# Optimization experiments

Hardware: AMD Instinct MI355X
Metric: run time of the kernel (lower is better)

The kernel has to match this reference:

```python
import jax, jax.numpy as jnp
import numpy as np

SIZE = 8
MAX_NOISY_RATIO = 0.1
MAX_WEIGHT_RATIO = 1.0


def setup_inputs() -> dict:
    key = jax.random.key(0)
    k1, k2, k3 = jax.random.split(key, 3)
    b, c, h, w = 32, 1, 128, 128
    H, W = h * SIZE, w * SIZE
    return {
        "dmap_conv": jax.random.uniform(k1, (b, c, h, w), jnp.float32),
        "dmap_tran": jax.random.uniform(k2, (b, c, h, w), jnp.float32),
        "gt_density": jax.random.uniform(k3, (b, c, H, W), jnp.float32),
        "process": 1,
    }


def reference(dmap_conv, dmap_tran, gt_density, process):
    b, c, h, w = dmap_conv.shape
    weight = MAX_WEIGHT_RATIO * process
    noisy_ratio = MAX_NOISY_RATIO * process

    # AvgPool2d(kernel=SIZE) * SIZE^2 == sum over non-overlapping SIZE x SIZE blocks
    gt = gt_density.reshape(b, c, h, SIZE, w, SIZE).sum(axis=(3, 5))  # [b,c,h,w]

    dc = dmap_conv.reshape(b, -1)  # [b, c*h*w]
    dt = dmap_tran.reshape(b, -1)
    dg = gt.reshape(b, -1)

    num = int(h * w * noisy_ratio)
    if num < 1:
        return jnp.sum((dc - dg) ** 2) + jnp.sum((dt - dg) ** 2)

    err_c = jnp.abs(dg - dc)
    err_t = jnp.abs(dg - dt)
    comb_c = weight * dc + (1.0 - weight) * dg
    comb_t = weight * dt + (1.0 - weight) * dg

    # threshold = num-th largest error per row (min of top-k)
    thr_c = jax.lax.top_k(err_c, num)[0][:, -1:]  # [b,1]
    sup_from_tran = jnp.where(err_c >= thr_c, comb_t, dg)
    mse_conv = jnp.sum((dc - sup_from_tran) ** 2)

    thr_t = jax.lax.top_k(err_t, num)[0][:, -1:]
    sup_from_conv = jnp.where(err_t >= thr_t, comb_c, dg)
    mse_tran = jnp.sum((dt - sup_from_conv) ** 2)

    return mse_conv + mse_tran
```

## Files before the change

kernel.cpp:

```cpp
#include <hip/hip_runtime.h>
#include <hip/hip_bf16.h>

#define B 32
#define HW 16384
#define NROW 128
#define POOL 8
#define GTW 1024
#define TOTAL (B * HW)
#define LOSS_BLOCKS 1024

__global__ __launch_bounds__(256) void pool_kernel(const float* __restrict__ gt,
                                                   float* __restrict__ dg) {
    int out = blockIdx.x * 256 + threadIdx.x;
    int b   = out >> 14;
    int rem = out & (HW - 1);
    int oi  = rem >> 7;
    int oj  = rem & (NROW - 1);
    const float* base = gt + ((size_t)b << 20) + (size_t)(oi * POOL) * GTW + oj * POOL;
    float s = 0.f;
#pragma unroll
    for (int r = 0; r < POOL; ++r) {
        const float4* p = reinterpret_cast<const float4*>(base + (size_t)r * GTW);
        float4 a = p[0];
        float4 c = p[1];
        s += a.x + a.y + a.z + a.w + c.x + c.y + c.z + c.w;
    }
    dg[out] = s;
}

__global__ __launch_bounds__(256) void select_kernel(const float* __restrict__ dc_all,
                                                     const float* __restrict__ dt_all,
                                                     const float* __restrict__ dg_all,
                                                     const int* __restrict__ process,
                                                     float* __restrict__ thr_out) {
    int b     = blockIdx.x >> 1;
    int which = blockIdx.x & 1;
    const float* dm = (which ? dt_all : dc_all) + (size_t)b * HW;
    const float* dg = dg_all + (size_t)b * HW;

    int p = process[0];
    int num = (int)(16384.0 * (0.1 * (double)p));
    if (num > HW) num = HW;

    int t = threadIdx.x;

    if (num < 1) {
        if (t == 0) thr_out[which * B + b] = __uint_as_float(0x7F800000u);
        return;
    }

    float e[64];
#pragma unroll
    for (int i = 0; i < 64; ++i) {
        int idx = i * 256 + t;
        e[i] = fabsf(dg[idx] - dm[idx]);
    }

    __shared__ unsigned s_lo, s_hi;
    __shared__ int s_cnt[4];
    if (t == 0) { s_lo = 0u; s_hi = 0x7F800000u; }
    __syncthreads();

    while (true) {
        unsigned lo = s_lo, hi = s_hi;
        if (hi - lo <= 1u) break;
        unsigned mid = lo + ((hi - lo) >> 1);
        float fmid = __uint_as_float(mid);
        int c = 0;
#pragma unroll
        for (int i = 0; i < 64; ++i) c += (e[i] >= fmid) ? 1 : 0;
#pragma unroll
        for (int off = 32; off > 0; off >>= 1) c += __shfl_down(c, off, 64);
        if ((t & 63) == 0) s_cnt[t >> 6] = c;
        __syncthreads();
        if (t == 0) {
            int tot = s_cnt[0] + s_cnt[1] + s_cnt[2] + s_cnt[3];
            if (tot >= num) s_lo = mid; else s_hi = mid;
        }
        __syncthreads();
    }

    if (t == 0) thr_out[which * B + b] = __uint_as_float(s_lo);
}

__global__ __launch_bounds__(256) void loss_kernel(const float* __restrict__ dc_all,
                                                   const float* __restrict__ dt_all,
                                                   const float* __restrict__ dg_all,
                                                   const int* __restrict__ process,
                                                   const float* __restrict__ thr,
                                                   double* __restrict__ part) {
    int p = process[0];
    int num = (int)(16384.0 * (0.1 * (double)p));
    float w = (float)(1.0 * (double)p);

    double acc = 0.0;
    for (int idx = blockIdx.x * 256 + threadIdx.x; idx < TOTAL; idx += LOSS_BLOCKS * 256) {
        int b = idx >> 14;
        float c = dc_all[idx];
        float t = dt_all[idx];
        float g = dg_all[idx];
        float d1, d2;
        if (num < 1) {
            d1 = c - g;
            d2 = t - g;
        } else {
            float ec = fabsf(g - c);
            float et = fabsf(g - t);
            float comb_c = w * c + (1.0f - w) * g;
            float comb_t = w * t + (1.0f - w) * g;
            float sup_c = (ec >= thr[b]) ? comb_t : g;
            float sup_t = (et >= thr[B + b]) ? comb_c : g;
            d1 = c - sup_c;
            d2 = t - sup_t;
        }
        acc += (double)(d1 * d1) + (double)(d2 * d2);
    }

    __shared__ double s_sum[4];
#pragma unroll
    for (int off = 32; off > 0; off >>= 1) acc += __shfl_down(acc, off, 64);
    int t = threadIdx.x;
    if ((t & 63) == 0) s_sum[t >> 6] = acc;
    __syncthreads();
    if (t == 0) part[blockIdx.x] = s_sum[0] + s_sum[1] + s_sum[2] + s_sum[3];
}

__global__ __launch_bounds__(256) void reduce_kernel(const double* __restrict__ part,
                                                     float* __restrict__ out) {
    int t = threadIdx.x;
    double acc = part[t] + part[t + 256] + part[t + 512] + part[t + 768];
#pragma unroll
    for (int off = 32; off > 0; off >>= 1) acc += __shfl_down(acc, off, 64);
    __shared__ double s_sum[4];
    if ((t & 63) == 0) s_sum[t >> 6] = acc;
    __syncthreads();
    if (t == 0) out[0] = (float)(s_sum[0] + s_sum[1] + s_sum[2] + s_sum[3]);
}

extern "C" void kernel_launch(void* const* d_in, const int* in_sizes, int n_in,
                              void* d_out, int out_size, void* d_ws, size_t ws_size,
                              hipStream_t stream) {
    const float* dmap_conv = (const float*)d_in[0];
    const float* dmap_tran = (const float*)d_in[1];
    const float* gt        = (const float*)d_in[2];
    const int*   process   = (const int*)d_in[3];
    float* out = (float*)d_out;

    char* ws = (char*)d_ws;
    float*  dg   = (float*)ws;
    float*  thr  = (float*)(ws + (size_t)TOTAL * sizeof(float));
    double* part = (double*)(ws + (size_t)TOTAL * sizeof(float) + 256);

    pool_kernel<<<TOTAL / 256, 256, 0, stream>>>(gt, dg);
    select_kernel<<<B * 2, 256, 0, stream>>>(dmap_conv, dmap_tran, dg, process, thr);
    loss_kernel<<<LOSS_BLOCKS, 256, 0, stream>>>(dmap_conv, dmap_tran, dg, process, thr, part);
    reduce_kernel<<<1, 256, 0, stream>>>(part, out);
}
```

Measured before the change: 224.2 us.

## Fuse threshold selection, loss and final reduction; narrow search range with 4-way bisection

Merges the select, loss and reduce kernels into one kernel of 64 blocks. Each block computes its row's threshold and then its half of the loss, and the partial sums are combined with double atomics plus a last-block counter. The threshold search now starts from the row's min and max error and splits the range four ways per pass, so fewer block-wide synchronisation rounds are needed. This removes two launches and a full reread of the data at low parallelism. In exchange the loss pass runs on only 64 blocks, and atomic double adds make the summation order nondeterministic.

```diff
diff --git a/kernel.cpp b/kernel.cpp
--- a/kernel.cpp
+++ b/kernel.cpp
@@ -7,11 +7,15 @@
 #define POOL 8
 #define GTW 1024
 #define TOTAL (B * HW)
-#define LOSS_BLOCKS 1024
+#define NBLK (B * 2)
+
 
 __global__ __launch_bounds__(256) void pool_kernel(const float* __restrict__ gt,
-                                                   float* __restrict__ dg) {
+                                                   float* __restrict__ dg,
+                                                   double* __restrict__ acc,
+                                                   unsigned* __restrict__ cnt) {
     int out = blockIdx.x * 256 + threadIdx.x;
+    if (out == 0) { *acc = 0.0; *cnt = 0u; }
     int b   = out >> 14;
     int rem = out & (HW - 1);
     int oi  = rem >> 7;
@@ -28,113 +32,140 @@
     dg[out] = s;
 }
 
-__global__ __launch_bounds__(256) void select_kernel(const float* __restrict__ dc_all,
-                                                     const float* __restrict__ dt_all,
-                                                     const float* __restrict__ dg_all,
-                                                     const int* __restrict__ process,
-                                                     float* __restrict__ thr_out) {
+__global__ __launch_bounds__(256) void selloss_kernel(const float* __restrict__ dc_all,
+                                                      const float* __restrict__ dt_all,
+                                                      const float* __restrict__ dg_all,
+                                                      const int* __restrict__ process,
+                                                      double* __restrict__ acc,
+                                                      unsigned* __restrict__ cnt,
+                                                      float* __restrict__ out) {
     int b     = blockIdx.x >> 1;
     int which = blockIdx.x & 1;
     const float* dm = (which ? dt_all : dc_all) + (size_t)b * HW;
+    const float* dq = (which ? dc_all : dt_all) + (size_t)b * HW;
     const float* dg = dg_all + (size_t)b * HW;
 
     int p = process[0];
     int num = (int)(16384.0 * (0.1 * (double)p));
     if (num > HW) num = HW;
+    float w = (float)(1.0 * (double)p);
 
     int t = threadIdx.x;
 
-    if (num < 1) {
-        if (t == 0) thr_out[which * B + b] = __uint_as_float(0x7F800000u);
-        return;
+    __shared__ unsigned s_lo, s_hi;
+    __shared__ unsigned long long s_pk[4];
+    __shared__ float s_mn[4], s_mx[4];
+    __shared__ double s_d[4];
+
+    float thr = __uint_as_float(0x7F800000u);
+
+    if (num >= 1) {
+        float e[64];
+#pragma unroll
+        for (int i = 0; i < 64; ++i) {
+            int idx = i * 256 + t;
+            e[i] = fabsf(dg[idx] - dm[idx]);
+        }
+
+        float mn = e[0], mx = e[0];
+#pragma unroll
+        for (int i = 1; i < 64; ++i) { mn = fminf(mn, e[i]); mx = fmaxf(mx, e[i]); }
+#pragma unroll
+        for (int off = 32; off > 0; off >>= 1) {
+            mn = fminf(mn, __shfl_down(mn, off, 64));
+            mx = fmaxf(mx, __shfl_down(mx, off, 64));
+        }
+        if ((t & 63) == 0) { s_mn[t >> 6] = mn; s_mx[t >> 6] = mx; }
+        __syncthreads();
+        if (t == 0) {
+            float a = fminf(fminf(s_mn[0], s_mn[1]), fminf(s_mn[2], s_mn[3]));
+            float z = fmaxf(fmaxf(s_mx[0], s_mx[1]), fmaxf(s_mx[2], s_mx[3]));
+            s_lo = __float_as_uint(a);
+            s_hi = __float_as_uint(z) + 1u;
+        }
+        __syncthreads();
+
+        unsigned lo, hi;
+        while (true) {
+            lo = s_lo; hi = s_hi;
+            unsigned r = hi - lo;
+            if (r <= 1u) break;
+            unsigned long long pk;
+            unsigned q = 0;
+            if (r >= 4u) {
+                q = r >> 2;
+                float m1 = __uint_as_float(lo + q);
+                float m2 = __uint_as_float(lo + 2u * q);
+                float m3 = __uint_as_float(lo + 3u * q);
+                unsigned c1 = 0, c2 = 0, c3 = 0;
+#pragma unroll
+                for (int i = 0; i < 64; ++i) {
+                    c1 += (e[i] >= m1);
+                    c2 += (e[i] >= m2);
+                    c3 += (e[i] >= m3);
+                }
+                pk = (unsigned long long)c1 | ((unsigned long long)c2 << 21) |
+                     ((unsigned long long)c3 << 42);
+            } else {
+                unsigned m = lo + (r >> 1);
+                float fm = __uint_as_float(m);
+                unsigned c = 0;
+#pragma unroll
+                for (int i = 0; i < 64; ++i) c += (e[i] >= fm);
+                pk = (unsigned long long)c;
+            }
+#pragma unroll
+            for (int off = 32; off > 0; off >>= 1) pk += __shfl_down(pk, off, 64);
+            if ((t & 63) == 0) s_pk[t >> 6] = pk;
+            __syncthreads();
+            if (t == 0) {
+                unsigned long long tot = s_pk[0] + s_pk[1] + s_pk[2] + s_pk[3];
+                if (r >= 4u) {
+                    int C1 = (int)(tot & 0x1FFFFFu);
+                    int C2 = (int)((tot >> 21) & 0x1FFFFFu);
+                    int C3 = (int)((tot >> 42) & 0x1FFFFFu);
+                    if      (C1 < num)  s_hi = lo + q;
+                    else if (C2 < num) { s_lo = lo + q;      s_hi = lo + 2u * q; }
+                    else if (C3 < num) { s_lo = lo + 2u * q; s_hi = lo + 3u * q; }
+                    else                s_lo = lo + 3u * q;
+                } else {
+                    unsigned m = lo + (r >> 1);
+                    if ((int)tot < num) s_hi = m; else s_lo = m;
+                }
+            }
+            __syncthreads();
+        }
+        thr = __uint_as_float(lo);
     }
 
-    float e[64];
-#pragma unroll
+    double lacc = 0.0;
+#pragma unroll 8
     for (int i = 0; i < 64; ++i) {
         int idx = i * 256 + t;
-        e[i] = fabsf(dg[idx] - dm[idx]);
+        float m_ = dm[idx];
+        float o_ = dq[idx];
+        float g  = dg[idx];
+        float err   = fabsf(g - m_);
+        float combo = w * o_ + (1.0f - w) * g;
+        float sup   = (err >= thr) ? combo : g;
+        float d     = m_ - sup;
+        lacc += (double)(d * d);
     }
 
-    __shared__ unsigned s_lo, s_hi;
-    __shared__ int s_cnt[4];
-    if (t == 0) { s_lo = 0u; s_hi = 0x7F800000u; }
+#pragma unroll
+    for (int off = 32; off > 0; off >>= 1) lacc += __shfl_down(lacc, off, 64);
+    if ((t & 63) == 0) s_d[t >> 6] = lacc;
     __syncthreads();
-
-    while (true) {
-        unsigned lo = s_lo, hi = s_hi;
-        if (hi - lo <= 1u) break;
-        unsigned mid = lo + ((hi - lo) >> 1);
-        float fmid = __uint_as_float(mid);
-        int c = 0;
-#pragma unroll
-        for (int i = 0; i < 64; ++i) c += (e[i] >= fmid) ? 1 : 0;
-#pragma unroll
-        for (int off = 32; off > 0; off >>= 1) c += __shfl_down(c, off, 64);
-        if ((t & 63) == 0) s_cnt[t >> 6] = c;
-        __syncthreads();
-        if (t == 0) {
-            int tot = s_cnt[0] + s_cnt[1] + s_cnt[2] + s_cnt[3];
-            if (tot >= num) s_lo = mid; else s_hi = mid;
+    if (t == 0) {
+        double tot = s_d[0] + s_d[1] + s_d[2] + s_d[3];
+        atomicAdd(acc, tot);
+        __threadfence();
+        unsigned old = atomicAdd(cnt, 1u);
+        if (old == NBLK - 1) {
+            double fin = atomicAdd(acc, 0.0);
+            out[0] = (float)fin;
         }
-        __syncthreads();
     }
-
-    if (t == 0) thr_out[which * B + b] = __uint_as_float(s_lo);
-}
-
-__global__ __launch_bounds__(256) void loss_kernel(const float* __restrict__ dc_all,
-                                                   const float* __restrict__ dt_all,
-                                                   const float* __restrict__ dg_all,
-                                                   const int* __restrict__ process,
-                                                   const float* __restrict__ thr,
-                                                   double* __restrict__ part) {
-    int p = process[0];
-    int num = (int)(16384.0 * (0.1 * (double)p));
-    float w = (float)(1.0 * (double)p);
-
-    double acc = 0.0;
-    for (int idx = blockIdx.x * 256 + threadIdx.x; idx < TOTAL; idx += LOSS_BLOCKS * 256) {
-        int b = idx >> 14;
-        float c = dc_all[idx];
-        float t = dt_all[idx];
-        float g = dg_all[idx];
-        float d1, d2;
-        if (num < 1) {
-            d1 = c - g;
-            d2 = t - g;
-        } else {
-            float ec = fabsf(g - c);
-            float et = fabsf(g - t);
-            float comb_c = w * c + (1.0f - w) * g;
-            float comb_t = w * t + (1.0f - w) * g;
-            float sup_c = (ec >= thr[b]) ? comb_t : g;
-            float sup_t = (et >= thr[B + b]) ? comb_c : g;
-            d1 = c - sup_c;
-            d2 = t - sup_t;
-        }
-        acc += (double)(d1 * d1) + (double)(d2 * d2);
-    }
-
-    __shared__ double s_sum[4];
-#pragma unroll
-    for (int off = 32; off > 0; off >>= 1) acc += __shfl_down(acc, off, 64);
-    int t = threadIdx.x;
-    if ((t & 63) == 0) s_sum[t >> 6] = acc;
-    __syncthreads();
-    if (t == 0) part[blockIdx.x] = s_sum[0] + s_sum[1] + s_sum[2] + s_sum[3];
-}
-
-__global__ __launch_bounds__(256) void reduce_kernel(const double* __restrict__ part,
-                                                     float* __restrict__ out) {
-    int t = threadIdx.x;
-    double acc = part[t] + part[t + 256] + part[t + 512] + part[t + 768];
-#pragma unroll
-    for (int off = 32; off > 0; off >>= 1) acc += __shfl_down(acc, off, 64);
-    __shared__ double s_sum[4];
-    if ((t & 63) == 0) s_sum[t >> 6] = acc;
-    __syncthreads();
-    if (t == 0) out[0] = (float)(s_sum[0] + s_sum[1] + s_sum[2] + s_sum[3]);
 }
 
 extern "C" void kernel_launch(void* const* d_in, const int* in_sizes, int n_in,
@@ -147,12 +178,10 @@
     float* out = (float*)d_out;
 
     char* ws = (char*)d_ws;
-    float*  dg   = (float*)ws;
-    float*  thr  = (float*)(ws + (size_t)TOTAL * sizeof(float));
-    double* part = (double*)(ws + (size_t)TOTAL * sizeof(float) + 256);
+    double*   acc = (double*)ws;
+    unsigned* cnt = (unsigned*)(ws + 8);
+    float*    dg  = (float*)(ws + 64);
 
-    pool_kernel<<<TOTAL / 256, 256, 0, stream>>>(gt, dg);
-    select_kernel<<<B * 2, 256, 0, stream>>>(dmap_conv, dmap_tran, dg, process, thr);
-    loss_kernel<<<LOSS_BLOCKS, 256, 0, stream>>>(dmap_conv, dmap_tran, dg, process, thr, part);
-    reduce_kernel<<<1, 256, 0, stream>>>(part, out);
+    pool_kernel<<<TOTAL / 256, 256, 0, stream>>>(gt, dg, acc, cnt);
+    selloss_kernel<<<NBLK, 256, 0, stream>>>(dmap_conv, dmap_tran, dg, process, acc, cnt, out);
 }
```

Result: no change. 226.1 us (+0.9%).
